# Performance work log

Measured on AMD Instinct MI355X. Metric: run time of the kernel, lower is better.

## Reference

```python
import jax, jax.numpy as jnp
import numpy as np


def _mlp(x, W1, b1, W2, b2):
    # Dropout layers are identity at inference (p=0.2 in train only).
    h = jax.nn.relu(jnp.einsum('bsi,ih->bsh', x, W1) + b1)
    return jax.nn.relu(jnp.einsum('bsh,hk->bsk', h, W2) + b2)


def setup_inputs() -> dict:
    key = jax.random.key(0)
    ks = jax.random.split(key, 4)
    B_, S, D_in, H = 32, 1024, 768, 1024
    A = jax.random.normal(ks[0], (B_, S, D_in), dtype=jnp.float32)
    B = jax.random.normal(ks[1], (B_, S, D_in), dtype=jnp.float32)
    W1 = jax.random.normal(ks[2], (D_in, H), dtype=jnp.float32) * (1.0 / np.sqrt(D_in))
    b1 = jnp.zeros((H,), dtype=jnp.float32)
    W2 = jax.random.normal(ks[3], (H, H), dtype=jnp.float32) * (1.0 / np.sqrt(H))
    b2 = jnp.zeros((H,), dtype=jnp.float32)
    return {"A": A, "B": B, "W1": W1, "b1": b1, "W2": W2, "b2": b2}


def reference(A, B, W1, b1, W2, b2):
    f_A = _mlp(A, W1, b1, W2, b2)           # [b, S, H]
    f_B = _mlp(B, W1, b1, W2, b2)           # [b, S, H]
    e = jnp.einsum('bih,bjh->bij', f_A, f_B)  # [b, S_A, S_B] unscaled scores
    beta = jnp.einsum('bij,bjd->bid', jax.nn.softmax(e, axis=-1), B)
    # alpha = softmax(e^T, -1) @ B  (note: B, exactly as in the source code)
    alpha = jnp.einsum('bji,bjd->bid', jax.nn.softmax(jnp.swapaxes(e, 1, 2), axis=-1), B)
    return (beta, alpha)
```

## Files before the change

kernel.cpp:

```cpp
#include <hip/hip_runtime.h>
#include <hip/hip_bf16.h>

typedef __attribute__((ext_vector_type(8))) short bf16x8;
typedef __attribute__((ext_vector_type(4))) float f32x4;

__device__ __forceinline__ unsigned short f2bf(float f) {
  union { float f; unsigned u; } v; v.f = f;
  unsigned r = v.u + 0x7FFFu + ((v.u >> 16) & 1u);
  return (unsigned short)(r >> 16);
}

__device__ __forceinline__ void gl_lds16(const void* g, void* l) {
  __builtin_amdgcn_global_load_lds(
      (__attribute__((address_space(1))) void*)(g),
      (__attribute__((address_space(3))) void*)(l), 16, 0, 0);
}

__global__ __launch_bounds__(256) void k_convert(const float* __restrict__ in,
                                                 unsigned short* __restrict__ out,
                                                 int n8) {
  int i = blockIdx.x * 256 + threadIdx.x;
  if (i >= n8) return;
  const float4* ip = (const float4*)in;
  float4 v0 = ip[2 * i], v1 = ip[2 * i + 1];
  ushort4 o0 = make_ushort4(f2bf(v0.x), f2bf(v0.y), f2bf(v0.z), f2bf(v0.w));
  ushort4 o1 = make_ushort4(f2bf(v1.x), f2bf(v1.y), f2bf(v1.z), f2bf(v1.w));
  ((ushort4*)out)[2 * i] = o0;
  ((ushort4*)out)[2 * i + 1] = o1;
}

template <typename OutT>
__global__ __launch_bounds__(256) void k_transpose(const float* __restrict__ in,
                                                   OutT* __restrict__ out,
                                                   int R, int C,
                                                   long inStride, long outStride) {
  __shared__ float tile[64][65];
  const float* ib = in + (long)blockIdx.z * inStride;
  OutT* ob = out + (long)blockIdx.z * outStride;
  int tc = blockIdx.x * 64;
  int tr = blockIdx.y * 64;
  int t = threadIdx.x;
  int lr = t >> 4;
  int lc = (t & 15) * 4;
#pragma unroll
  for (int rr = 0; rr < 64; rr += 16) {
    float4 v = *(const float4*)&ib[(long)(tr + rr + lr) * C + tc + lc];
    tile[rr + lr][lc + 0] = v.x;
    tile[rr + lr][lc + 1] = v.y;
    tile[rr + lr][lc + 2] = v.z;
    tile[rr + lr][lc + 3] = v.w;
  }
  __syncthreads();
#pragma unroll
  for (int ii = 0; ii < 64; ii += 16) {
    int i = ii + lr;
    if constexpr (sizeof(OutT) == 2) {
      ushort4 w = make_ushort4(f2bf(tile[lc + 0][i]), f2bf(tile[lc + 1][i]),
                               f2bf(tile[lc + 2][i]), f2bf(tile[lc + 3][i]));
      *(ushort4*)&ob[(long)(tc + i) * R + tr + lc] = w;
    } else {
      float4 w = make_float4(tile[lc + 0][i], tile[lc + 1][i],
                             tile[lc + 2][i], tile[lc + 3][i]);
      *(float4*)&ob[(long)(tc + i) * R + tr + lc] = w;
    }
  }
}

__global__ __launch_bounds__(256) void k_convtrans_B(const float* __restrict__ in,
                                                     unsigned short* __restrict__ xbf,
                                                     unsigned short* __restrict__ bt) {
  __shared__ float tile[64][65];
  const int bz = blockIdx.z;
  const float* ib = in + (long)bz * 786432L;
  unsigned short* ob = bt + (long)bz * 786432L;
  int tc = blockIdx.x * 64;
  int tr = blockIdx.y * 64;
  int t = threadIdx.x;
  int lr = t >> 4;
  int lc = (t & 15) * 4;
#pragma unroll
  for (int rr = 0; rr < 64; rr += 16) {
    float4 v = *(const float4*)&ib[(long)(tr + rr + lr) * 768 + tc + lc];
    tile[rr + lr][lc + 0] = v.x;
    tile[rr + lr][lc + 1] = v.y;
    tile[rr + lr][lc + 2] = v.z;
    tile[rr + lr][lc + 3] = v.w;
    ushort4 w = make_ushort4(f2bf(v.x), f2bf(v.y), f2bf(v.z), f2bf(v.w));
    *(ushort4*)&xbf[(long)(32768 + bz * 1024 + tr + rr + lr) * 768 + tc + lc] = w;
  }
  __syncthreads();
#pragma unroll
  for (int ii = 0; ii < 64; ii += 16) {
    int i = ii + lr;
    ushort4 w = make_ushort4(f2bf(tile[lc + 0][i]), f2bf(tile[lc + 1][i]),
                             f2bf(tile[lc + 2][i]), f2bf(tile[lc + 3][i]));
    *(ushort4*)&ob[(long)(tc + i) * 1024 + tr + lc] = w;
  }
}

__global__ __launch_bounds__(256) void k_statcombine(
    const float* __restrict__ rowPM, const float* __restrict__ rowPS,
    const float* __restrict__ colPM, const float* __restrict__ colPS,
    float* __restrict__ rowM, float* __restrict__ rowIS,
    float* __restrict__ colM, float* __restrict__ colIS) {
  int idx = blockIdx.x * 256 + threadIdx.x;
  if (idx < 32768) {
    int z = idx >> 10, i = idx & 1023;
    float mv[4], sv[4];
    float m = -3.4e38f;
#pragma unroll
    for (int k = 0; k < 4; ++k) {
      mv[k] = rowPM[((long)z * 4 + k) * 1024 + i];
      sv[k] = rowPS[((long)z * 4 + k) * 1024 + i];
      m = fmaxf(m, mv[k]);
    }
    float s = 0.f;
#pragma unroll
    for (int k = 0; k < 4; ++k) s += sv[k] * __expf(mv[k] - m);
    rowM[idx] = m;
    rowIS[idx] = 1.0f / s;
  } else {
    int j = idx - 32768;
    int z = j >> 10, c = j & 1023;
    float mv[8], sv[8];
    float m = -3.4e38f;
#pragma unroll
    for (int k = 0; k < 8; ++k) {
      mv[k] = colPM[((long)z * 8 + k) * 1024 + c];
      sv[k] = colPS[((long)z * 8 + k) * 1024 + c];
      m = fmaxf(m, mv[k]);
    }
    float s = 0.f;
#pragma unroll
    for (int k = 0; k < 8; ++k) s += sv[k] * __expf(mv[k] - m);
    colM[j] = m;
    colIS[j] = 1.0f / s;
  }
}

__global__ __launch_bounds__(256) void k_softmax(const float* __restrict__ E,
                                                 unsigned short* __restrict__ P,
                                                 unsigned short* __restrict__ P2,
                                                 const float* __restrict__ rowM,
                                                 const float* __restrict__ rowIS,
                                                 const float* __restrict__ colM,
                                                 const float* __restrict__ colIS) {
  long row = blockIdx.x;
  int t = threadIdx.x;
  float4 v = *(const float4*)&E[row * 1024 + t * 4];
  float rm = rowM[row], ri = rowIS[row];
  *(ushort4*)&P[row * 1024 + t * 4] =
      make_ushort4(f2bf(__expf(v.x - rm) * ri), f2bf(__expf(v.y - rm) * ri),
                   f2bf(__expf(v.z - rm) * ri), f2bf(__expf(v.w - rm) * ri));
  long cb = (row >> 10) * 1024 + t * 4;
  float4 cm = *(const float4*)&colM[cb];
  float4 ci = *(const float4*)&colIS[cb];
  *(ushort4*)&P2[row * 1024 + t * 4] =
      make_ushort4(f2bf(__expf(v.x - cm.x) * ci.x), f2bf(__expf(v.y - cm.y) * ci.y),
                   f2bf(__expf(v.z - cm.z) * ci.z), f2bf(__expf(v.w - cm.w) * ci.w));
}

template <bool BIAS_RELU, bool OUT_BF16, bool STATS>
__global__ __launch_bounds__(256, 2) void k_gemm_bt(
    const unsigned short* __restrict__ A, long lda, long aBatch,
    const unsigned short* __restrict__ A2,
    const unsigned short* __restrict__ Bt, long ldb, long bBatch,
    void* __restrict__ C, void* __restrict__ C2, long ldc, long cBatch,
    const float* __restrict__ bias, int K, int zsplit,
    float* __restrict__ rowPM, float* __restrict__ rowPS,
    float* __restrict__ colPM, float* __restrict__ colPS) {
  __shared__ unsigned short As[128 * 64];
  __shared__ unsigned short Bs[256 * 64];
  const int t = threadIdx.x;
  const int w = t >> 6, l = t & 63;
  const int lr = l & 15, lh = l >> 4;
  const int wm = w >> 1, wn = w & 1;

  const int gx = gridDim.x, gy = gridDim.y;
  const int nwg = gx * gy * gridDim.z;
  const int hw = blockIdx.x + gx * (blockIdx.y + gy * blockIdx.z);
  const int q = nwg >> 3;
  const int logical = (hw & 7) * q + (hw >> 3);
  const int bx = logical % gx;
  const int rem = logical / gx;
  const int by = rem % gy;
  int bz = rem / gy;

  const unsigned short* Abase = A;
  void* Cbase = C;
  if (bz >= zsplit) { Abase = A2; Cbase = C2; bz -= zsplit; }

  const long m0 = (long)by * 128;
  const long n0 = (long)bx * 256;
  const unsigned short* Ab = Abase + (long)bz * aBatch;
  const unsigned short* Bb = Bt + (long)bz * bBatch;

  const int srow = t >> 3;
  const int sc16 = (t & 7) ^ (srow & 7);
  const int scol = sc16 * 8;
  const unsigned short* ag = Ab + (m0 + srow) * lda + scol;
  const unsigned short* bg = Bb + (n0 + srow) * ldb + scol;
  unsigned short* al = &As[srow * 64 + (t & 7) * 8];
  unsigned short* bl = &Bs[srow * 64 + (t & 7) * 8];

  f32x4 acc[4][8];
#pragma unroll
  for (int i = 0; i < 4; ++i)
#pragma unroll
    for (int j = 0; j < 8; ++j) acc[i][j] = (f32x4){0.f, 0.f, 0.f, 0.f};

  for (int k0 = 0; k0 < K; k0 += 64) {
#pragma unroll
    for (int j = 0; j < 4; ++j)
      gl_lds16(ag + (long)(j * 32) * lda + k0, al + j * 2048);
#pragma unroll
    for (int j = 0; j < 8; ++j)
      gl_lds16(bg + (long)(j * 32) * ldb + k0, bl + j * 2048);
    __syncthreads();
#pragma unroll
    for (int kk = 0; kk < 2; ++kk) {
      const int rsw = ((kk * 4 + lh) ^ (lr & 7)) * 8;
      bf16x8 af[4], bfr[8];
#pragma unroll
      for (int m = 0; m < 4; ++m)
        af[m] = *(const bf16x8*)&As[(wm * 64 + m * 16 + lr) * 64 + rsw];
#pragma unroll
      for (int n = 0; n < 8; ++n)
        bfr[n] = *(const bf16x8*)&Bs[(wn * 128 + n * 16 + lr) * 64 + rsw];
#pragma unroll
      for (int m = 0; m < 4; ++m)
#pragma unroll
        for (int n = 0; n < 8; ++n)
          acc[m][n] = __builtin_amdgcn_mfma_f32_16x16x32_bf16(af[m], bfr[n], acc[m][n], 0, 0, 0);
    }
    __syncthreads();
  }

  const long crow = m0 + wm * 64;
  const long ccol = n0 + wn * 128;
#pragma unroll
  for (int n = 0; n < 8; ++n) {
    const long col = ccol + n * 16 + lr;
    float bv = 0.f;
    if constexpr (BIAS_RELU) bv = bias[col];
#pragma unroll
    for (int m = 0; m < 4; ++m) {
      f32x4 v = acc[m][n];
#pragma unroll
      for (int r = 0; r < 4; ++r) {
        const long rrow = crow + m * 16 + lh * 4 + r;
        float x = v[r];
        if constexpr (BIAS_RELU) x = fmaxf(x + bv, 0.f);
        if constexpr (OUT_BF16)
          ((unsigned short*)Cbase)[(long)bz * cBatch + rrow * ldc + col] = f2bf(x);
        else
          ((float*)Cbase)[(long)bz * cBatch + rrow * ldc + col] = x;
      }
    }
  }

  if constexpr (STATS) {
    float* ldsRM = (float*)As;
    float* ldsRS = (float*)As + 256;
    float* ldsCM = (float*)Bs;
    float* ldsCS = (float*)Bs + 512;
#pragma unroll
    for (int m = 0; m < 4; ++m) {
#pragma unroll
      for (int r = 0; r < 4; ++r) {
        float lm = acc[m][0][r];
#pragma unroll
        for (int n = 1; n < 8; ++n) lm = fmaxf(lm, acc[m][n][r]);
#pragma unroll
        for (int o = 1; o < 16; o <<= 1) lm = fmaxf(lm, __shfl_xor(lm, o));
        float ls = 0.f;
#pragma unroll
        for (int n = 0; n < 8; ++n) ls += __expf(acc[m][n][r] - lm);
#pragma unroll
        for (int o = 1; o < 16; o <<= 1) ls += __shfl_xor(ls, o);
        if (lr == 0) {
          int row = wm * 64 + m * 16 + lh * 4 + r;
          ldsRM[row * 2 + wn] = lm;
          ldsRS[row * 2 + wn] = ls;
        }
      }
    }
#pragma unroll
    for (int n = 0; n < 8; ++n) {
      float lm = acc[0][n][0];
#pragma unroll
      for (int m = 0; m < 4; ++m)
#pragma unroll
        for (int r = 0; r < 4; ++r) lm = fmaxf(lm, acc[m][n][r]);
#pragma unroll
      for (int o = 16; o < 64; o <<= 1) lm = fmaxf(lm, __shfl_xor(lm, o));
      float ls = 0.f;
#pragma unroll
      for (int m = 0; m < 4; ++m)
#pragma unroll
        for (int r = 0; r < 4; ++r) ls += __expf(acc[m][n][r] - lm);
#pragma unroll
      for (int o = 16; o < 64; o <<= 1) ls += __shfl_xor(ls, o);
      if (lh == 0) {
        int col = wn * 128 + n * 16 + lr;
        ldsCM[col * 2 + wm] = lm;
        ldsCS[col * 2 + wm] = ls;
      }
    }
    __syncthreads();
    if (t < 128) {
      float m0v = ldsRM[t * 2], m1v = ldsRM[t * 2 + 1];
      float s0v = ldsRS[t * 2], s1v = ldsRS[t * 2 + 1];
      float mm = fmaxf(m0v, m1v);
      float ss = s0v * __expf(m0v - mm) + s1v * __expf(m1v - mm);
      long o = ((long)bz * 4 + bx) * 1024 + by * 128 + t;
      rowPM[o] = mm;
      rowPS[o] = ss;
    }
    {
      float m0v = ldsCM[t * 2], m1v = ldsCM[t * 2 + 1];
      float s0v = ldsCS[t * 2], s1v = ldsCS[t * 2 + 1];
      float mm = fmaxf(m0v, m1v);
      float ss = s0v * __expf(m0v - mm) + s1v * __expf(m1v - mm);
      long o = ((long)bz * 8 + by) * 1024 + bx * 256 + t;
      colPM[o] = mm;
      colPS[o] = ss;
    }
  }
}

extern "C" void kernel_launch(void* const* d_in, const int* in_sizes, int n_in,
                              void* d_out, int out_size, void* d_ws, size_t ws_size,
                              hipStream_t stream) {
  const float* A_in = (const float*)d_in[0];
  const float* B_in = (const float*)d_in[1];
  const float* W1 = (const float*)d_in[2];
  const float* b1 = (const float*)d_in[3];
  const float* W2 = (const float*)d_in[4];
  const float* b2 = (const float*)d_in[5];

  char* ws = (char*)d_ws;
  unsigned short* Xbf  = (unsigned short*)(ws + 0L);
  unsigned short* H    = (unsigned short*)(ws + 100663296L);
  unsigned short* F    = (unsigned short*)(ws + 234881024L);
  unsigned short* BinT = (unsigned short*)(ws + 369098752L);
  unsigned short* W1T  = (unsigned short*)(ws + 419430400L);
  unsigned short* W2T  = (unsigned short*)(ws + 421003264L);
  unsigned short* P    = (unsigned short*)(ws + 0L);
  unsigned short* P2   = (unsigned short*)(ws + 234881024L);
  float* rowPM = (float*)(ws + 100663296L);
  float* rowPS = (float*)(ws + 100663296L + 524288L);
  float* colPM = (float*)(ws + 100663296L + 1048576L);
  float* colPS = (float*)(ws + 100663296L + 2097152L);
  float* rowM  = (float*)(ws + 100663296L + 3145728L);
  float* rowIS = (float*)(ws + 100663296L + 3276800L);
  float* colM  = (float*)(ws + 100663296L + 3407872L);
  float* colIS = (float*)(ws + 100663296L + 3538944L);
  float* E  = (float*)d_out;
  float* beta = (float*)d_out;
  float* alpha = (float*)d_out + 25165824L;
  const int NOSPLIT = 1 << 30;

  k_convert<<<12288, 256, 0, stream>>>(A_in, Xbf, 3145728);
  k_convtrans_B<<<dim3(12, 16, 32), 256, 0, stream>>>(B_in, Xbf, BinT);
  k_transpose<unsigned short><<<dim3(16, 12, 1), 256, 0, stream>>>(W1, W1T, 768, 1024, 0, 0);
  k_transpose<unsigned short><<<dim3(16, 16, 1), 256, 0, stream>>>(W2, W2T, 1024, 1024, 0, 0);

  k_gemm_bt<true, true, false><<<dim3(4, 512, 1), 256, 0, stream>>>(
      Xbf, 768, 0, nullptr, W1T, 768, 0, (void*)H, nullptr, 1024, 0, b1, 768, NOSPLIT,
      nullptr, nullptr, nullptr, nullptr);
  k_gemm_bt<true, true, false><<<dim3(4, 512, 1), 256, 0, stream>>>(
      H, 1024, 0, nullptr, W2T, 1024, 0, (void*)F, nullptr, 1024, 0, b2, 1024, NOSPLIT,
      nullptr, nullptr, nullptr, nullptr);

  k_gemm_bt<false, false, true><<<dim3(4, 8, 32), 256, 0, stream>>>(
      F, 1024, 1048576L, nullptr, F + 33554432L, 1024, 1048576L, (void*)E, nullptr,
      1024, 1048576L, nullptr, 1024, NOSPLIT, rowPM, rowPS, colPM, colPS);

  k_statcombine<<<256, 256, 0, stream>>>(rowPM, rowPS, colPM, colPS,
                                         rowM, rowIS, colM, colIS);
  k_softmax<<<32768, 256, 0, stream>>>(E, P, P2, rowM, rowIS, colM, colIS);

  k_gemm_bt<false, false, false><<<dim3(3, 8, 64), 256, 0, stream>>>(
      P, 1024, 1048576L, P2, BinT, 1024, 786432L, (void*)beta, (void*)alpha,
      768, 786432L, nullptr, 1024, 32, nullptr, nullptr, nullptr, nullptr);
}
```

Measured before the change: 644.0 us.

## Fuse softmax normalization into final GEMM A-operand load from fp32 scores

Removes the standalone softmax kernel and the bf16 P/P2 buffers. The final batched GEMM now reads fp32 scores directly, applies exp and the row or column max and inverse-sum on the fly, and writes bf16 values into the swizzled LDS tile. This is meant to save the round trip of writing and re-reading the probability matrices and one kernel launch. In exchange, each A tile becomes a synchronous fp32 register load with exp work inside the main loop. The exp is recomputed once per output column tile, and twice as many A bytes are read per tile.

```diff
diff --git a/kernel.cpp b/kernel.cpp
--- a/kernel.cpp
+++ b/kernel.cpp
@@ -138,37 +138,15 @@
   }
 }
 
-__global__ __launch_bounds__(256) void k_softmax(const float* __restrict__ E,
-                                                 unsigned short* __restrict__ P,
-                                                 unsigned short* __restrict__ P2,
-                                                 const float* __restrict__ rowM,
-                                                 const float* __restrict__ rowIS,
-                                                 const float* __restrict__ colM,
-                                                 const float* __restrict__ colIS) {
-  long row = blockIdx.x;
-  int t = threadIdx.x;
-  float4 v = *(const float4*)&E[row * 1024 + t * 4];
-  float rm = rowM[row], ri = rowIS[row];
-  *(ushort4*)&P[row * 1024 + t * 4] =
-      make_ushort4(f2bf(__expf(v.x - rm) * ri), f2bf(__expf(v.y - rm) * ri),
-                   f2bf(__expf(v.z - rm) * ri), f2bf(__expf(v.w - rm) * ri));
-  long cb = (row >> 10) * 1024 + t * 4;
-  float4 cm = *(const float4*)&colM[cb];
-  float4 ci = *(const float4*)&colIS[cb];
-  *(ushort4*)&P2[row * 1024 + t * 4] =
-      make_ushort4(f2bf(__expf(v.x - cm.x) * ci.x), f2bf(__expf(v.y - cm.y) * ci.y),
-                   f2bf(__expf(v.z - cm.z) * ci.z), f2bf(__expf(v.w - cm.w) * ci.w));
-}
-
-template <bool BIAS_RELU, bool OUT_BF16, bool STATS>
+template <bool BIAS_RELU, bool OUT_BF16, bool STATS, int SMODE>
 __global__ __launch_bounds__(256, 2) void k_gemm_bt(
     const unsigned short* __restrict__ A, long lda, long aBatch,
     const unsigned short* __restrict__ A2,
     const unsigned short* __restrict__ Bt, long ldb, long bBatch,
     void* __restrict__ C, void* __restrict__ C2, long ldc, long cBatch,
     const float* __restrict__ bias, int K, int zsplit,
-    float* __restrict__ rowPM, float* __restrict__ rowPS,
-    float* __restrict__ colPM, float* __restrict__ colPS) {
+    float* __restrict__ sA, float* __restrict__ sB,
+    float* __restrict__ sC, float* __restrict__ sD) {
   __shared__ unsigned short As[128 * 64];
   __shared__ unsigned short Bs[256 * 64];
   const int t = threadIdx.x;
@@ -188,7 +166,8 @@
 
   const unsigned short* Abase = A;
   void* Cbase = C;
-  if (bz >= zsplit) { Abase = A2; Cbase = C2; bz -= zsplit; }
+  bool alphaP = false;
+  if (bz >= zsplit) { Abase = A2; Cbase = C2; bz -= zsplit; alphaP = true; }
 
   const long m0 = (long)by * 128;
   const long n0 = (long)bx * 256;
@@ -196,12 +175,27 @@
   const unsigned short* Bb = Bt + (long)bz * bBatch;
 
   const int srow = t >> 3;
-  const int sc16 = (t & 7) ^ (srow & 7);
+  const int c8 = t & 7;
+  const int sc16 = c8 ^ (srow & 7);
   const int scol = sc16 * 8;
   const unsigned short* ag = Ab + (m0 + srow) * lda + scol;
   const unsigned short* bg = Bb + (n0 + srow) * ldb + scol;
-  unsigned short* al = &As[srow * 64 + (t & 7) * 8];
-  unsigned short* bl = &Bs[srow * 64 + (t & 7) * 8];
+  unsigned short* al = &As[srow * 64 + c8 * 8];
+  unsigned short* bl = &Bs[srow * 64 + c8 * 8];
+
+  const float* Epan = nullptr;
+  float rmv[4], riv[4];
+  if constexpr (SMODE == 1) {
+    Epan = (const float*)Abase + (long)bz * 1048576L;
+    if (!alphaP) {
+#pragma unroll
+      for (int j = 0; j < 4; ++j) {
+        long r = (long)bz * 1024 + m0 + srow + j * 32;
+        rmv[j] = sA[r];
+        riv[j] = sB[r];
+      }
+    }
+  }
 
   f32x4 acc[4][8];
 #pragma unroll
@@ -210,12 +204,47 @@
     for (int j = 0; j < 8; ++j) acc[i][j] = (f32x4){0.f, 0.f, 0.f, 0.f};
 
   for (int k0 = 0; k0 < K; k0 += 64) {
-#pragma unroll
-    for (int j = 0; j < 4; ++j)
-      gl_lds16(ag + (long)(j * 32) * lda + k0, al + j * 2048);
 #pragma unroll
     for (int j = 0; j < 8; ++j)
       gl_lds16(bg + (long)(j * 32) * ldb + k0, bl + j * 2048);
+    if constexpr (SMODE == 0) {
+#pragma unroll
+      for (int j = 0; j < 4; ++j)
+        gl_lds16(ag + (long)(j * 32) * lda + k0, al + j * 2048);
+    } else {
+      float sub[8], mul[8];
+      if (alphaP) {
+        long cbase = (long)bz * 1024 + k0 + c8 * 8;
+        float4 cm0 = *(const float4*)&sC[cbase];
+        float4 cm1 = *(const float4*)&sC[cbase + 4];
+        float4 ci0 = *(const float4*)&sD[cbase];
+        float4 ci1 = *(const float4*)&sD[cbase + 4];
+        sub[0] = cm0.x; sub[1] = cm0.y; sub[2] = cm0.z; sub[3] = cm0.w;
+        sub[4] = cm1.x; sub[5] = cm1.y; sub[6] = cm1.z; sub[7] = cm1.w;
+        mul[0] = ci0.x; mul[1] = ci0.y; mul[2] = ci0.z; mul[3] = ci0.w;
+        mul[4] = ci1.x; mul[5] = ci1.y; mul[6] = ci1.z; mul[7] = ci1.w;
+      }
+#pragma unroll
+      for (int j = 0; j < 4; ++j) {
+        const int row = srow + j * 32;
+        const float* src = Epan + (long)(m0 + row) * 1024 + k0 + c8 * 8;
+        float4 e0 = *(const float4*)src;
+        float4 e1 = *(const float4*)(src + 4);
+        float ev[8] = {e0.x, e0.y, e0.z, e0.w, e1.x, e1.y, e1.z, e1.w};
+        union { unsigned short us[8]; int4 qd; } pk;
+        if (alphaP) {
+#pragma unroll
+          for (int e = 0; e < 8; ++e)
+            pk.us[e] = f2bf(__expf(ev[e] - sub[e]) * mul[e]);
+        } else {
+          float rm = rmv[j], ri = riv[j];
+#pragma unroll
+          for (int e = 0; e < 8; ++e)
+            pk.us[e] = f2bf(__expf(ev[e] - rm) * ri);
+        }
+        *(int4*)&As[row * 64 + sc16 * 8] = pk.qd;
+      }
+    }
     __syncthreads();
 #pragma unroll
     for (int kk = 0; kk < 2; ++kk) {
@@ -314,8 +343,8 @@
       float mm = fmaxf(m0v, m1v);
       float ss = s0v * __expf(m0v - mm) + s1v * __expf(m1v - mm);
       long o = ((long)bz * 4 + bx) * 1024 + by * 128 + t;
-      rowPM[o] = mm;
-      rowPS[o] = ss;
+      sA[o] = mm;
+      sB[o] = ss;
     }
     {
       float m0v = ldsCM[t * 2], m1v = ldsCM[t * 2 + 1];
@@ -323,8 +352,8 @@
       float mm = fmaxf(m0v, m1v);
       float ss = s0v * __expf(m0v - mm) + s1v * __expf(m1v - mm);
       long o = ((long)bz * 8 + by) * 1024 + bx * 256 + t;
-      colPM[o] = mm;
-      colPS[o] = ss;
+      sC[o] = mm;
+      sD[o] = ss;
     }
   }
 }
@@ -346,17 +375,15 @@
   unsigned short* BinT = (unsigned short*)(ws + 369098752L);
   unsigned short* W1T  = (unsigned short*)(ws + 419430400L);
   unsigned short* W2T  = (unsigned short*)(ws + 421003264L);
-  unsigned short* P    = (unsigned short*)(ws + 0L);
-  unsigned short* P2   = (unsigned short*)(ws + 234881024L);
-  float* rowPM = (float*)(ws + 100663296L);
-  float* rowPS = (float*)(ws + 100663296L + 524288L);
-  float* colPM = (float*)(ws + 100663296L + 1048576L);
-  float* colPS = (float*)(ws + 100663296L + 2097152L);
-  float* rowM  = (float*)(ws + 100663296L + 3145728L);
-  float* rowIS = (float*)(ws + 100663296L + 3276800L);
-  float* colM  = (float*)(ws + 100663296L + 3407872L);
-  float* colIS = (float*)(ws + 100663296L + 3538944L);
-  float* E  = (float*)d_out;
+  float* E = (float*)(ws + 0L);
+  float* rowPM = (float*)(ws + 146800640L);
+  float* rowPS = (float*)(ws + 146800640L + 524288L);
+  float* colPM = (float*)(ws + 146800640L + 1048576L);
+  float* colPS = (float*)(ws + 146800640L + 2097152L);
+  float* rowM  = (float*)(ws + 146800640L + 3145728L);
+  float* rowIS = (float*)(ws + 146800640L + 3276800L);
+  float* colM  = (float*)(ws + 146800640L + 3407872L);
+  float* colIS = (float*)(ws + 146800640L + 3538944L);
   float* beta = (float*)d_out;
   float* alpha = (float*)d_out + 25165824L;
   const int NOSPLIT = 1 << 30;
@@ -366,22 +393,22 @@
   k_transpose<unsigned short><<<dim3(16, 12, 1), 256, 0, stream>>>(W1, W1T, 768, 1024, 0, 0);
   k_transpose<unsigned short><<<dim3(16, 16, 1), 256, 0, stream>>>(W2, W2T, 1024, 1024, 0, 0);
 
-  k_gemm_bt<true, true, false><<<dim3(4, 512, 1), 256, 0, stream>>>(
+  k_gemm_bt<true, true, false, 0><<<dim3(4, 512, 1), 256, 0, stream>>>(
       Xbf, 768, 0, nullptr, W1T, 768, 0, (void*)H, nullptr, 1024, 0, b1, 768, NOSPLIT,
       nullptr, nullptr, nullptr, nullptr);
-  k_gemm_bt<true, true, false><<<dim3(4, 512, 1), 256, 0, stream>>>(
+  k_gemm_bt<true, true, false, 0><<<dim3(4, 512, 1), 256, 0, stream>>>(
       H, 1024, 0, nullptr, W2T, 1024, 0, (void*)F, nullptr, 1024, 0, b2, 1024, NOSPLIT,
       nullptr, nullptr, nullptr, nullptr);
 
-  k_gemm_bt<false, false, true><<<dim3(4, 8, 32), 256, 0, stream>>>(
+  k_gemm_bt<false, false, true, 0><<<dim3(4, 8, 32), 256, 0, stream>>>(
       F, 1024, 1048576L, nullptr, F + 33554432L, 1024, 1048576L, (void*)E, nullptr,
       1024, 1048576L, nullptr, 1024, NOSPLIT, rowPM, rowPS, colPM, colPS);
 
   k_statcombine<<<256, 256, 0, stream>>>(rowPM, rowPS, colPM, colPS,
                                          rowM, rowIS, colM, colIS);
-  k_softmax<<<32768, 256, 0, stream>>>(E, P, P2, rowM, rowIS, colM, colIS);
-
-  k_gemm_bt<false, false, false><<<dim3(3, 8, 64), 256, 0, stream>>>(
-      P, 1024, 1048576L, P2, BinT, 1024, 786432L, (void*)beta, (void*)alpha,
-      768, 786432L, nullptr, 1024, 32, nullptr, nullptr, nullptr, nullptr);
-}
+
+  k_gemm_bt<false, false, false, 1><<<dim3(3, 8, 64), 256, 0, stream>>>(
+      (const unsigned short*)E, 1024, 1048576L, (const unsigned short*)E,
+      BinT, 1024, 786432L, (void*)beta, (void*)alpha,
+      768, 786432L, nullptr, 1024, 32, rowM, rowIS, colM, colIS);
+}
```

After: 668.8 us. +3.9%, slower.

## Double-buffer B tile and prefetch next K-tile during MFMA compute

Applied to the files above, without the earlier changes.

The GEMM main loop now keeps two LDS buffers for the B tile. A fragments are read into registers first, then the next K-tile's global-to-LDS loads are issued before the MFMAs on the current tile run, so memory latency overlaps with compute. This raises LDS use from 48KB to 80KB per block, which may cut occupancy below the requested 2 blocks per CU. It also adds an extra barrier per iteration.

```diff
diff --git a/kernel.cpp b/kernel.cpp
--- a/kernel.cpp
+++ b/kernel.cpp
@@ -170,7 +170,7 @@
     float* __restrict__ rowPM, float* __restrict__ rowPS,
     float* __restrict__ colPM, float* __restrict__ colPS) {
   __shared__ unsigned short As[128 * 64];
-  __shared__ unsigned short Bs[256 * 64];
+  __shared__ unsigned short Bs[2][256 * 64];
   const int t = threadIdx.x;
   const int w = t >> 6, l = t & 63;
   const int lr = l & 15, lh = l >> 4;
@@ -201,7 +201,7 @@
   const unsigned short* ag = Ab + (m0 + srow) * lda + scol;
   const unsigned short* bg = Bb + (n0 + srow) * ldb + scol;
   unsigned short* al = &As[srow * 64 + (t & 7) * 8];
-  unsigned short* bl = &Bs[srow * 64 + (t & 7) * 8];
+  const int bloff = srow * 64 + (t & 7) * 8;
 
   f32x4 acc[4][8];
 #pragma unroll
@@ -209,29 +209,48 @@
 #pragma unroll
     for (int j = 0; j < 8; ++j) acc[i][j] = (f32x4){0.f, 0.f, 0.f, 0.f};
 
-  for (int k0 = 0; k0 < K; k0 += 64) {
-#pragma unroll
-    for (int j = 0; j < 4; ++j)
-      gl_lds16(ag + (long)(j * 32) * lda + k0, al + j * 2048);
-#pragma unroll
-    for (int j = 0; j < 8; ++j)
-      gl_lds16(bg + (long)(j * 32) * ldb + k0, bl + j * 2048);
-    __syncthreads();
+#pragma unroll
+  for (int j = 0; j < 4; ++j)
+    gl_lds16(ag + (long)(j * 32) * lda, al + j * 2048);
+#pragma unroll
+  for (int j = 0; j < 8; ++j)
+    gl_lds16(bg + (long)(j * 32) * ldb, &Bs[0][bloff] + j * 2048);
+  __syncthreads();
+
+  const int NT = K >> 6;
+  for (int tt = 0; tt < NT; ++tt) {
+    const int cur = tt & 1;
+    bf16x8 af[4][2];
 #pragma unroll
     for (int kk = 0; kk < 2; ++kk) {
       const int rsw = ((kk * 4 + lh) ^ (lr & 7)) * 8;
-      bf16x8 af[4], bfr[8];
 #pragma unroll
       for (int m = 0; m < 4; ++m)
-        af[m] = *(const bf16x8*)&As[(wm * 64 + m * 16 + lr) * 64 + rsw];
+        af[m][kk] = *(const bf16x8*)&As[(wm * 64 + m * 16 + lr) * 64 + rsw];
+    }
+    __syncthreads();
+    if (tt + 1 < NT) {
+      const int kn = (tt + 1) << 6;
+#pragma unroll
+      for (int j = 0; j < 4; ++j)
+        gl_lds16(ag + (long)(j * 32) * lda + kn, al + j * 2048);
+      unsigned short* bln = &Bs[cur ^ 1][bloff];
+#pragma unroll
+      for (int j = 0; j < 8; ++j)
+        gl_lds16(bg + (long)(j * 32) * ldb + kn, bln + j * 2048);
+    }
+#pragma unroll
+    for (int kk = 0; kk < 2; ++kk) {
+      const int rsw = ((kk * 4 + lh) ^ (lr & 7)) * 8;
+      bf16x8 bfr[8];
 #pragma unroll
       for (int n = 0; n < 8; ++n)
-        bfr[n] = *(const bf16x8*)&Bs[(wn * 128 + n * 16 + lr) * 64 + rsw];
+        bfr[n] = *(const bf16x8*)&Bs[cur][(wn * 128 + n * 16 + lr) * 64 + rsw];
 #pragma unroll
       for (int m = 0; m < 4; ++m)
 #pragma unroll
         for (int n = 0; n < 8; ++n)
-          acc[m][n] = __builtin_amdgcn_mfma_f32_16x16x32_bf16(af[m], bfr[n], acc[m][n], 0, 0, 0);
+          acc[m][n] = __builtin_amdgcn_mfma_f32_16x16x32_bf16(af[m][kk], bfr[n], acc[m][n], 0, 0, 0);
     }
     __syncthreads();
   }
@@ -262,8 +281,8 @@
   if constexpr (STATS) {
     float* ldsRM = (float*)As;
     float* ldsRS = (float*)As + 256;
-    float* ldsCM = (float*)Bs;
-    float* ldsCS = (float*)Bs + 512;
+    float* ldsCM = (float*)&Bs[0][0];
+    float* ldsCS = (float*)&Bs[0][0] + 512;
 #pragma unroll
     for (int m = 0; m < 4; ++m) {
 #pragma unroll
```

After: 646.0 us. Within noise of the previous version (+0.3%).
